# Performance work log

Measured on AMD Instinct MI355X. Metric: run time of the kernel, lower is better.

The kernel has to match this reference:

```python
import jax, jax.numpy as jnp
import numpy as np

D_MODEL = 1024
N_HEADS = 16
D_HEAD = D_MODEL // N_HEADS


def setup_inputs() -> dict:
    key = jax.random.key(0)
    ks = jax.random.split(key, 9)
    s = 1.0 / np.sqrt(D_MODEL)
    x = jax.random.normal(ks[0], (2, 2048, D_MODEL), dtype=jnp.float32)
    # torch nn.Linear stores weight [out, in]; we store [in, out] for x @ W
    Wq = jax.random.uniform(ks[1], (D_MODEL, D_MODEL), jnp.float32, -s, s)
    bq = jax.random.uniform(ks[2], (D_MODEL,), jnp.float32, -s, s)
    Wk = jax.random.uniform(ks[3], (D_MODEL, D_MODEL), jnp.float32, -s, s)
    bk = jax.random.uniform(ks[4], (D_MODEL,), jnp.float32, -s, s)
    Wv = jax.random.uniform(ks[5], (D_MODEL, D_MODEL), jnp.float32, -s, s)
    bv = jax.random.uniform(ks[6], (D_MODEL,), jnp.float32, -s, s)
    Wo = jax.random.uniform(ks[7], (D_MODEL, D_MODEL), jnp.float32, -s, s)
    bo = jax.random.uniform(ks[8], (D_MODEL,), jnp.float32, -s, s)
    return {"x": x, "Wq": Wq, "bq": bq, "Wk": Wk, "bk": bk,
            "Wv": Wv, "bv": bv, "Wo": Wo, "bo": bo}


def reference(x, Wq, bq, Wk, bk, Wv, bv, Wo, bo):
    B, S, _ = x.shape
    # project and split heads: [B, H, S, Dh]
    def split(t):
        return t.reshape(B, S, N_HEADS, D_HEAD).transpose(0, 2, 1, 3)
    Q = split(x @ Wq + bq)
    K = split(x @ Wk + bk)
    V = split(x @ Wv + bv)
    scale = 1.0 / jnp.sqrt(jnp.asarray(D_HEAD, x.dtype))
    scores = jnp.einsum('bhqd,bhkd->bhqk', Q, K) * scale  # [B,H,S,S]
    attn = jax.nn.softmax(scores, axis=-1)
    out = jnp.einsum('bhqk,bhkd->bhqd', attn, V)  # [B,H,S,Dh]
    out = out.transpose(0, 2, 1, 3).reshape(B, S, D_MODEL)
    return out @ Wo + bo
```

## Files before the change

kernel.cpp:

```cpp
#include <hip/hip_runtime.h>
#include <hip/hip_bf16.h>
#include <cmath>

#define D_MODEL 1024
#define N_HEADS 16
#define D_HEAD  64
#define BATCH   2
#define SEQ     2048
#define M_TOT   (BATCH*SEQ)
#define NELT    ((size_t)M_TOT * D_MODEL)

typedef __attribute__((ext_vector_type(8))) short short8;
typedef __attribute__((ext_vector_type(4))) float f32x4;

#define QSCALE (0.125f * 1.44269504088896f)

static __device__ __forceinline__ ushort f2bf(float f) {
    __hip_bfloat16 h = __float2bfloat16(f);
    return *reinterpret_cast<ushort*>(&h);
}

static __device__ __forceinline__ float exp2_raw(float x) {
    return __builtin_amdgcn_exp2f(x);
}

static __device__ __forceinline__ void gload_lds16(const void* g, void* l) {
    __builtin_amdgcn_global_load_lds((const __attribute__((address_space(1))) unsigned*)g,
                                     (__attribute__((address_space(3))) unsigned*)l,
                                     16, 0, 0);
}

__global__ __launch_bounds__(256)
void prep_kernel(const float* __restrict__ x,
                 const float* __restrict__ W0, const float* __restrict__ W1,
                 const float* __restrict__ W2, const float* __restrict__ W3,
                 ushort* __restrict__ xb, ushort* __restrict__ Wt0)
{
    __shared__ float Ts[64][65];
    const int z = blockIdx.z;
    const int t = threadIdx.x;

    if (z == 4) {
        const int slab = blockIdx.y * 16 + blockIdx.x;
#pragma unroll
        for (int u = 0; u < 16; ++u) {
            const int i = slab * 4096 + u * 256 + t;
            const float4 v = ((const float4*)x)[i];
            ushort4 uo;
            uo.x = f2bf(v.x); uo.y = f2bf(v.y); uo.z = f2bf(v.z); uo.w = f2bf(v.w);
            ((ushort4*)xb)[i] = uo;
        }
        return;
    }

    const float* W = (z == 0) ? W0 : (z == 1) ? W1 : (z == 2) ? W2 : W3;
    ushort* Wt = Wt0 + (size_t)z * D_MODEL * D_MODEL;

    const int n0 = blockIdx.x * 64;
    const int k0 = blockIdx.y * 64;
    const int rr = t >> 4;
    const int c4 = (t & 15) * 4;

#pragma unroll
    for (int i = 0; i < 4; ++i) {
        const int r = rr + i * 16;
        const float4 v = *(const float4*)&W[(size_t)(k0 + r) * D_MODEL + n0 + c4];
        Ts[r][c4 + 0] = v.x; Ts[r][c4 + 1] = v.y;
        Ts[r][c4 + 2] = v.z; Ts[r][c4 + 3] = v.w;
    }
    __syncthreads();
#pragma unroll
    for (int i = 0; i < 4; ++i) {
        const int nn = rr + i * 16;
        ushort4 u;
        u.x = f2bf(Ts[c4 + 0][nn]); u.y = f2bf(Ts[c4 + 1][nn]);
        u.z = f2bf(Ts[c4 + 2][nn]); u.w = f2bf(Ts[c4 + 3][nn]);
        *(ushort4*)&Wt[(size_t)(n0 + nn) * D_MODEL + k0 + c4] = u;
    }
}

__global__ __launch_bounds__(256)
void gemm_qkv_mfma(const ushort* __restrict__ A, const ushort* __restrict__ Bt,
                   const float* __restrict__ bq, const float* __restrict__ bk,
                   const float* __restrict__ bv, ushort* __restrict__ QKV)
{
    __shared__ ushort SH[2 * 128 * 64];
    ushort* As = SH;
    ushort* Bs = SH + 128 * 64;

    const int t    = threadIdx.x;
    const int lane = t & 63;
    const int w    = t >> 6;
    const int wr   = w >> 1;
    const int wc   = w & 1;
    const int l16  = lane & 15;
    const int g    = lane >> 4;
    const int m0   = blockIdx.y * 128;
    const int n0   = blockIdx.x * 128;

    f32x4 acc[4][4];
#pragma unroll
    for (int i = 0; i < 4; ++i)
#pragma unroll
        for (int j = 0; j < 4; ++j) acc[i][j] = f32x4{0.f, 0.f, 0.f, 0.f};

    for (int kt = 0; kt < D_MODEL; kt += 64) {
        __syncthreads();
        const ushort* Ag = A  + (size_t)m0 * D_MODEL + kt;
        const ushort* Bg = Bt + (size_t)n0 * D_MODEL + kt;
#pragma unroll
        for (int it = 0; it < 4; ++it) {
            const int b   = (it * 256 + t) * 16;
            const int row = b >> 7;
            const int src = (b & 127) ^ ((row & 7) << 4);
            const int lof = (it * 256 + (t & ~63)) * 8;
            gload_lds16(Ag + (size_t)row * D_MODEL + (src >> 1), As + lof);
            gload_lds16(Bg + (size_t)row * D_MODEL + (src >> 1), Bs + lof);
        }
        __syncthreads();

#pragma unroll
        for (int kh = 0; kh < 2; ++kh) {
            short8 a[4], bfr[4];
#pragma unroll
            for (int fm = 0; fm < 4; ++fm) {
                const int row  = wr * 64 + fm * 16 + l16;
                const int byte = row * 128 + (((kh << 6) | (g << 4)) ^ ((row & 7) << 4));
                a[fm] = *(const short8*)((const char*)As + byte);
            }
#pragma unroll
            for (int fn = 0; fn < 4; ++fn) {
                const int row  = wc * 64 + fn * 16 + l16;
                const int byte = row * 128 + (((kh << 6) | (g << 4)) ^ ((row & 7) << 4));
                bfr[fn] = *(const short8*)((const char*)Bs + byte);
            }
#pragma unroll
            for (int fm = 0; fm < 4; ++fm)
#pragma unroll
                for (int fn = 0; fn < 4; ++fn)
                    acc[fm][fn] = __builtin_amdgcn_mfma_f32_16x16x32_bf16(a[fm], bfr[fn], acc[fm][fn], 0, 0, 0);
        }
    }

    const int proj = n0 >> 10;

    if (proj == 2) {
        __syncthreads();
#pragma unroll
        for (int fm = 0; fm < 4; ++fm) {
            const int ml = wr * 64 + fm * 16 + g * 4;
#pragma unroll
            for (int fn = 0; fn < 4; ++fn) {
                const int nnl = wc * 64 + fn * 16 + l16;
                const float bn = bv[(n0 & 1023) + nnl];
                ushort4 pk;
                pk.x = f2bf(acc[fm][fn][0] + bn);
                pk.y = f2bf(acc[fm][fn][1] + bn);
                pk.z = f2bf(acc[fm][fn][2] + bn);
                pk.w = f2bf(acc[fm][fn][3] + bn);
                *(ushort4*)((char*)SH + nnl * 256 + ((ml * 2) ^ ((nnl & 15) << 4))) = pk;
            }
        }
        __syncthreads();
        const int bb  = m0 >> 11;
        const int sA0 = m0 & (SEQ - 1);
        const int ch  = t & 15;
#pragma unroll
        for (int pass = 0; pass < 8; ++pass) {
            const int rr = pass * 16 + (t >> 4);
            const int nn = (n0 & 1023) + rr;
            const int h  = nn >> 6;
            const int dh = nn & 63;
            const short8 v = *(const short8*)((const char*)SH + rr * 256 +
                                              ((ch * 16) ^ ((rr & 15) << 4)));
            *(short8*)&QKV[2 * NELT + (((size_t)(bb * N_HEADS + h)) * D_HEAD + dh) * SEQ
                           + sA0 + ch * 8] = v;
        }
        return;
    }

#pragma unroll
    for (int fm = 0; fm < 4; ++fm) {
        const int mb  = m0 + wr * 64 + fm * 16 + g * 4;
        const int bb  = mb >> 11;
        const int sA  = mb & (SEQ - 1);
#pragma unroll
        for (int fn = 0; fn < 4; ++fn) {
            const int n  = n0 + wc * 64 + fn * 16 + l16;
            const int nn = n & 1023;
            const int h  = nn >> 6;
            const int dh = nn & 63;
            const float bn = (proj == 0) ? bq[nn] : bk[nn];
            const float sc = (proj == 0) ? QSCALE : 1.0f;
            ushort* outp = QKV + (size_t)proj * NELT;
#pragma unroll
            for (int r = 0; r < 4; ++r) {
                const float c = (acc[fm][fn][r] + bn) * sc;
                outp[(((size_t)(bb * N_HEADS + h)) * SEQ + sA + r) * D_HEAD + dh] = f2bf(c);
            }
        }
    }
}

__global__ __launch_bounds__(256)
void gemm_out_mfma(const ushort* __restrict__ A, const ushort* __restrict__ Bt,
                   const float* __restrict__ bias, float* __restrict__ outp)
{
    __shared__ ushort As[64 * 64];
    __shared__ ushort Bs[128 * 64];

    const int t    = threadIdx.x;
    const int lane = t & 63;
    const int w    = t >> 6;
    const int l16  = lane & 15;
    const int g    = lane >> 4;
    const int m0   = blockIdx.y * 64;
    const int n0   = blockIdx.x * 128;

    f32x4 acc[4][2];
#pragma unroll
    for (int i = 0; i < 4; ++i)
#pragma unroll
        for (int j = 0; j < 2; ++j) acc[i][j] = f32x4{0.f, 0.f, 0.f, 0.f};

    for (int kt = 0; kt < D_MODEL; kt += 64) {
        __syncthreads();
        const ushort* Ag = A  + (size_t)m0 * D_MODEL + kt;
        const ushort* Bg = Bt + (size_t)n0 * D_MODEL + kt;
#pragma unroll
        for (int it = 0; it < 2; ++it) {
            const int b   = (it * 256 + t) * 16;
            const int row = b >> 7;
            const int src = (b & 127) ^ ((row & 7) << 4);
            const int lof = (it * 256 + (t & ~63)) * 8;
            gload_lds16(Ag + (size_t)row * D_MODEL + (src >> 1), As + lof);
        }
#pragma unroll
        for (int it = 0; it < 4; ++it) {
            const int b   = (it * 256 + t) * 16;
            const int row = b >> 7;
            const int src = (b & 127) ^ ((row & 7) << 4);
            const int lof = (it * 256 + (t & ~63)) * 8;
            gload_lds16(Bg + (size_t)row * D_MODEL + (src >> 1), Bs + lof);
        }
        __syncthreads();

#pragma unroll
        for (int kh = 0; kh < 2; ++kh) {
            short8 a[4], bfr[2];
#pragma unroll
            for (int fm = 0; fm < 4; ++fm) {
                const int row  = fm * 16 + l16;
                const int byte = row * 128 + (((kh << 6) | (g << 4)) ^ ((row & 7) << 4));
                a[fm] = *(const short8*)((const char*)As + byte);
            }
#pragma unroll
            for (int fn = 0; fn < 2; ++fn) {
                const int row  = w * 32 + fn * 16 + l16;
                const int byte = row * 128 + (((kh << 6) | (g << 4)) ^ ((row & 7) << 4));
                bfr[fn] = *(const short8*)((const char*)Bs + byte);
            }
#pragma unroll
            for (int fm = 0; fm < 4; ++fm)
#pragma unroll
                for (int fn = 0; fn < 2; ++fn)
                    acc[fm][fn] = __builtin_amdgcn_mfma_f32_16x16x32_bf16(a[fm], bfr[fn], acc[fm][fn], 0, 0, 0);
        }
    }

#pragma unroll
    for (int fm = 0; fm < 4; ++fm) {
        const int mb = m0 + fm * 16 + g * 4;
#pragma unroll
        for (int fn = 0; fn < 2; ++fn) {
            const int n  = n0 + w * 32 + fn * 16 + l16;
            const float bn = bias[n];
#pragma unroll
            for (int r = 0; r < 4; ++r)
                outp[(size_t)(mb + r) * D_MODEL + n] = acc[fm][fn][r] + bn;
        }
    }
}

__global__ __launch_bounds__(256)
void flash_attn_mfma(const ushort* __restrict__ Q, const ushort* __restrict__ K,
                     const ushort* __restrict__ Vt, ushort* __restrict__ AO)
{
    __shared__ ushort Kl[2][128 * 64];
    __shared__ ushort Vl[2][64 * 128];
    __shared__ ushort Ps[4][16 * 64];

    const int t    = threadIdx.x;
    const int w    = t >> 6;
    const int lane = t & 63;
    const int l16  = lane & 15;
    const int g    = lane >> 4;
    const int qt   = blockIdx.x;
    const int bh   = blockIdx.y;

    const size_t qkbase = (size_t)bh * SEQ * D_HEAD;
    const ushort* Vg0 = Vt + (size_t)bh * D_HEAD * SEQ;

    short8 qf[2][2];
#pragma unroll
    for (int tt = 0; tt < 2; ++tt) {
        const int q0 = qt * 128 + w * 32 + tt * 16;
        const ushort* qp = Q + qkbase + (size_t)(q0 + l16) * D_HEAD + g * 8;
        qf[tt][0] = *(const short8*)(qp);
        qf[tt][1] = *(const short8*)(qp + 32);
    }

    f32x4 o[2][4];
    float m_r[2], l_r[2];
#pragma unroll
    for (int tt = 0; tt < 2; ++tt) {
        m_r[tt] = -INFINITY; l_r[tt] = 0.f;
#pragma unroll
        for (int d = 0; d < 4; ++d) o[tt][d] = f32x4{0.f, 0.f, 0.f, 0.f};
    }

    auto stage = [&](int ktile, int b) {
        const ushort* Kg = K + qkbase + (size_t)(ktile * 128) * D_HEAD;
        const ushort* Vg = Vg0 + ktile * 128;
#pragma unroll
        for (int it = 0; it < 4; ++it) {
            const int bb   = (it * 256 + t) * 16;
            const int lof  = (it * 256 + (t & ~63)) * 8;
            const int rowK = bb >> 7;
            const int srcK = (bb & 127) ^ ((rowK & 7) << 4);
            gload_lds16(Kg + (size_t)rowK * D_HEAD + (srcK >> 1), &Kl[b][lof]);
            const int rowV = bb >> 8;
            const int srcV = (bb & 255) ^ ((rowV & 15) << 4);
            gload_lds16(Vg + (size_t)rowV * SEQ + (srcV >> 1), &Vl[b][lof]);
        }
    };

    stage(0, 0);
    __syncthreads();

    const int NT = SEQ / 128;
    for (int kt = 0; kt < NT; ++kt) {
        const int buf = kt & 1;
        if (kt + 1 < NT) stage(kt + 1, buf ^ 1);

#pragma unroll
        for (int h2 = 0; h2 < 2; ++h2) {
            short8 kf[4][2];
#pragma unroll
            for (int nt = 0; nt < 4; ++nt) {
                const int row = h2 * 64 + nt * 16 + l16;
#pragma unroll
                for (int ks = 0; ks < 2; ++ks) {
                    const int byte = row * 128 + (((ks * 64) | (g * 16)) ^ ((row & 7) << 4));
                    kf[nt][ks] = *(const short8*)((const char*)&Kl[buf][0] + byte);
                }
            }

            short8 vf[4][2];
#pragma unroll
            for (int dt = 0; dt < 4; ++dt) {
                const int row = dt * 16 + l16;
#pragma unroll
                for (int ks = 0; ks < 2; ++ks) {
                    const int byte = row * 256 + ((h2 * 128 + ks * 64 + g * 16) ^ ((row & 15) << 4));
                    vf[dt][ks] = *(const short8*)((const char*)&Vl[buf][0] + byte);
                }
            }

            f32x4 st[2][4];
#pragma unroll
            for (int tt = 0; tt < 2; ++tt)
#pragma unroll
                for (int nt = 0; nt < 4; ++nt) {
                    f32x4 a = f32x4{0.f, 0.f, 0.f, 0.f};
                    a = __builtin_amdgcn_mfma_f32_16x16x32_bf16(kf[nt][0], qf[tt][0], a, 0, 0, 0);
                    a = __builtin_amdgcn_mfma_f32_16x16x32_bf16(kf[nt][1], qf[tt][1], a, 0, 0, 0);
                    st[tt][nt] = a;
                }

#pragma unroll
            for (int tt = 0; tt < 2; ++tt) {
                float pmax = st[tt][0][0];
#pragma unroll
                for (int nt = 0; nt < 4; ++nt)
#pragma unroll
                    for (int r = 0; r < 4; ++r) pmax = fmaxf(pmax, st[tt][nt][r]);
                pmax = fmaxf(pmax, __shfl_xor(pmax, 16, 64));
                pmax = fmaxf(pmax, __shfl_xor(pmax, 32, 64));

                if (__any(pmax - m_r[tt] > 8.f)) {
                    const float mnew  = fmaxf(m_r[tt], pmax);
                    const float alpha = exp2_raw(m_r[tt] - mnew);
                    m_r[tt] = mnew;
                    l_r[tt] *= alpha;
                    float ar[4];
#pragma unroll
                    for (int r = 0; r < 4; ++r) ar[r] = __shfl(alpha, g * 4 + r, 64);
#pragma unroll
                    for (int dt = 0; dt < 4; ++dt)
#pragma unroll
                        for (int r = 0; r < 4; ++r) o[tt][dt][r] *= ar[r];
                }

                float rs = 0.f;
#pragma unroll
                for (int nt = 0; nt < 4; ++nt) {
                    ushort4 pk;
#pragma unroll
                    for (int r = 0; r < 4; ++r) {
                        const float p = exp2_raw(st[tt][nt][r] - m_r[tt]);
                        rs += p;
                        ((ushort*)&pk)[r] = f2bf(p);
                    }
                    const int pb = (nt * 32 + g * 8) ^ ((l16 & 7) << 4);
                    *(ushort4*)((char*)&Ps[w][0] + l16 * 128 + pb) = pk;
                }
                rs += __shfl_xor(rs, 16, 64);
                rs += __shfl_xor(rs, 32, 64);
                l_r[tt] += rs;

#pragma unroll
                for (int ks = 0; ks < 2; ++ks) {
                    const int rb = (ks * 64 + g * 16) ^ ((l16 & 7) << 4);
                    const short8 pf = *(const short8*)((const char*)&Ps[w][0] + l16 * 128 + rb);
#pragma unroll
                    for (int dt = 0; dt < 4; ++dt)
                        o[tt][dt] = __builtin_amdgcn_mfma_f32_16x16x32_bf16(pf, vf[dt][ks], o[tt][dt], 0, 0, 0);
                }
            }
        }

        __syncthreads();
    }

    const int b = bh >> 4;
    const int h = bh & 15;
#pragma unroll
    for (int tt = 0; tt < 2; ++tt) {
        const int q0 = qt * 128 + w * 32 + tt * 16;
        float lr_row[4];
#pragma unroll
        for (int r = 0; r < 4; ++r) lr_row[r] = __shfl(l_r[tt], g * 4 + r, 64);
#pragma unroll
        for (int r = 0; r < 4; ++r) {
            const float inv = 1.f / lr_row[r];
            const size_t row = (size_t)b * SEQ + q0 + g * 4 + r;
#pragma unroll
            for (int dt = 0; dt < 4; ++dt)
                AO[row * D_MODEL + h * D_HEAD + dt * 16 + l16] = f2bf(o[tt][dt][r] * inv);
        }
    }
}

extern "C" void kernel_launch(void* const* d_in, const int* in_sizes, int n_in,
                              void* d_out, int out_size, void* d_ws, size_t ws_size,
                              hipStream_t stream)
{
    const float* x  = (const float*)d_in[0];
    const float* Wq = (const float*)d_in[1];
    const float* bq = (const float*)d_in[2];
    const float* Wk = (const float*)d_in[3];
    const float* bk = (const float*)d_in[4];
    const float* Wv = (const float*)d_in[5];
    const float* bv = (const float*)d_in[6];
    const float* Wo = (const float*)d_in[7];
    const float* bo = (const float*)d_in[8];
    float* out = (float*)d_out;

    const size_t WELT = (size_t)D_MODEL * D_MODEL;
    ushort* xb  = (ushort*)d_ws;
    ushort* Wqt = xb + NELT;
    ushort* Wot = Wqt + 3 * WELT;
    ushort* Qb  = xb + 2 * NELT;
    ushort* Kb  = Qb + NELT;
    ushort* Vtb = Kb + NELT;
    ushort* AOb = xb + 5 * NELT;

    prep_kernel<<<dim3(D_MODEL / 64, D_MODEL / 64, 5), 256, 0, stream>>>(x, Wq, Wk, Wv, Wo, xb, Wqt);
    gemm_qkv_mfma<<<dim3(3 * D_MODEL / 128, M_TOT / 128), 256, 0, stream>>>(xb, Wqt, bq, bk, bv, Qb);
    flash_attn_mfma<<<dim3(SEQ / 128, BATCH * N_HEADS), 256, 0, stream>>>(Qb, Kb, Vtb, AOb);
    gemm_out_mfma<<<dim3(D_MODEL / 128, M_TOT / 64), 256, 0, stream>>>(AOb, Wot, bo, out);
}
```

Before: 127.8 us.

## Stage Q/K epilogue through LDS for vectorized stores; remap attention blocks per XCD

The QKV GEMM epilogue for Q and K now writes the scaled, biased bf16 results into a padded shared-memory tile, then issues 16-byte vectorized global stores per row instead of scattered 2-byte stores. The flash-attention launch becomes a 1D grid of 512 blocks whose index is remapped so that consecutive blocks round-robined across the 8 XCDs share the same batch-head. This is meant to improve L2 reuse of K/V within each XCD. The change costs an extra LDS round-trip and barrier in the epilogue and a slightly larger shared buffer.

```diff
diff --git a/kernel.cpp b/kernel.cpp
--- a/kernel.cpp
+++ b/kernel.cpp
@@ -84,7 +84,7 @@
                    const float* __restrict__ bq, const float* __restrict__ bk,
                    const float* __restrict__ bv, ushort* __restrict__ QKV)
 {
-    __shared__ ushort SH[2 * 128 * 64];
+    __shared__ ushort SH[128 * 136];
     ushort* As = SH;
     ushort* Bs = SH + 128 * 64;
 
@@ -179,25 +179,34 @@
         return;
     }
 
+    __syncthreads();
+    const float sc = (proj == 0) ? QSCALE : 1.0f;
 #pragma unroll
     for (int fm = 0; fm < 4; ++fm) {
-        const int mb  = m0 + wr * 64 + fm * 16 + g * 4;
-        const int bb  = mb >> 11;
-        const int sA  = mb & (SEQ - 1);
+        const int mlb = wr * 64 + fm * 16 + g * 4;
 #pragma unroll
         for (int fn = 0; fn < 4; ++fn) {
-            const int n  = n0 + wc * 64 + fn * 16 + l16;
-            const int nn = n & 1023;
+            const int nnl = wc * 64 + fn * 16 + l16;
+            const float bn = (proj == 0) ? bq[(n0 & 1023) + nnl] : bk[(n0 & 1023) + nnl];
+#pragma unroll
+            for (int r = 0; r < 4; ++r)
+                SH[(mlb + r) * 136 + nnl] = f2bf((acc[fm][fn][r] + bn) * sc);
+        }
+    }
+    __syncthreads();
+    {
+        ushort* outp = QKV + (size_t)proj * NELT;
+        const int bb  = m0 >> 11;
+        const int sA0 = m0 & (SEQ - 1);
+        const int ch  = t & 15;
+#pragma unroll
+        for (int pass = 0; pass < 8; ++pass) {
+            const int rr = pass * 16 + (t >> 4);
+            const int nn = (n0 & 1023) + ch * 8;
             const int h  = nn >> 6;
             const int dh = nn & 63;
-            const float bn = (proj == 0) ? bq[nn] : bk[nn];
-            const float sc = (proj == 0) ? QSCALE : 1.0f;
-            ushort* outp = QKV + (size_t)proj * NELT;
-#pragma unroll
-            for (int r = 0; r < 4; ++r) {
-                const float c = (acc[fm][fn][r] + bn) * sc;
-                outp[(((size_t)(bb * N_HEADS + h)) * SEQ + sA + r) * D_HEAD + dh] = f2bf(c);
-            }
+            const short8 v = *(const short8*)&SH[rr * 136 + ch * 8];
+            *(short8*)&outp[(((size_t)(bb * N_HEADS + h)) * SEQ + sA0 + rr) * D_HEAD + dh] = v;
         }
     }
 }
@@ -295,8 +304,10 @@
     const int lane = t & 63;
     const int l16  = lane & 15;
     const int g    = lane >> 4;
-    const int qt   = blockIdx.x;
-    const int bh   = blockIdx.y;
+    const int i    = blockIdx.x;
+    const int slot = i >> 3;
+    const int bh   = (i & 7) * 4 + (slot >> 4);
+    const int qt   = slot & 15;
 
     const size_t qkbase = (size_t)bh * SEQ * D_HEAD;
     const ushort* Vg0 = Vt + (size_t)bh * D_HEAD * SEQ;
@@ -478,6 +489,6 @@
 
     prep_kernel<<<dim3(D_MODEL / 64, D_MODEL / 64, 5), 256, 0, stream>>>(x, Wq, Wk, Wv, Wo, xb, Wqt);
     gemm_qkv_mfma<<<dim3(3 * D_MODEL / 128, M_TOT / 128), 256, 0, stream>>>(xb, Wqt, bq, bk, bv, Qb);
-    flash_attn_mfma<<<dim3(SEQ / 128, BATCH * N_HEADS), 256, 0, stream>>>(Qb, Kb, Vtb, AOb);
+    flash_attn_mfma<<<dim3(512), 256, 0, stream>>>(Qb, Kb, Vtb, AOb);
     gemm_out_mfma<<<dim3(D_MODEL / 128, M_TOT / 64), 256, 0, stream>>>(AOb, Wot, bo, out);
 }
```

Measured after the change: 125.1 us, median of 3. 2.1% less time.
